# Kernel tuning notes

Measured on AMD Instinct MI355X. Metric: run time of the kernel, lower is better.

The kernel has to match this reference:

```python
import jax, jax.numpy as jnp
import numpy as np

B, T, F, H, OUT = 256, 256, 128, 1024, 128


def setup_inputs() -> dict:
    key = jax.random.key(0)
    ks = jax.random.split(key, 6)
    s_ih = 1.0 / np.sqrt(H)
    return {
        "x": jax.random.normal(ks[0], (B, T, F), dtype=jnp.float32),
        "h0": jnp.zeros((B, H), dtype=jnp.float32),
        "c0": jnp.zeros((B, H), dtype=jnp.float32),
        "W_ih": jax.random.normal(ks[1], (4 * H, F), dtype=jnp.float32) * s_ih,
        "W_hh": jax.random.normal(ks[2], (4 * H, H), dtype=jnp.float32) * s_ih,
        "b_ih": jax.random.normal(ks[3], (4 * H,), dtype=jnp.float32) * s_ih,
        "b_hh": jax.random.normal(ks[4], (4 * H,), dtype=jnp.float32) * s_ih,
        "W_fc": jax.random.normal(ks[5], (OUT, H), dtype=jnp.float32) * s_ih,
        "b_fc": jnp.zeros((OUT,), dtype=jnp.float32),
    }


def _lstm_scan(x, h0, c0, W_ih, W_hh, b_ih, b_hh):
    # Precompute input projections for all timesteps: [T, B, 4H]
    x_t = jnp.swapaxes(x, 0, 1)  # [T, B, F]
    x_proj = jnp.einsum('tbf,gf->tbg', x_t, W_ih) + b_ih + b_hh

    def step(carry, xp):
        h, c = carry
        gates = xp + h @ W_hh.T  # [B, 4H]
        i, f, g, o = jnp.split(gates, 4, axis=-1)  # PyTorch LSTMCell gate order
        i = jax.nn.sigmoid(i)
        f = jax.nn.sigmoid(f)
        g = jnp.tanh(g)
        o = jax.nn.sigmoid(o)
        c = f * c + i * g
        h = o * jnp.tanh(c)
        return (h, c), None

    (h, c), _ = jax.lax.scan(step, (h0, c0), x_proj)
    return h, c


def reference(x, h0, c0, W_ih, W_hh, b_ih, b_hh, W_fc, b_fc):
    h, c = _lstm_scan(x, h0, c0, W_ih, W_hh, b_ih, b_hh)
    sig_out = jax.nn.sigmoid(h)
    # Dropout is identity in eval/reference mode
    return sig_out @ W_fc.T + b_fc  # [B, OUT]
```

## Files before the change

kernel.cpp:

```cpp
#include <hip/hip_runtime.h>


typedef _Float16 f16x8 __attribute__((ext_vector_type(8)));
typedef float f32x4 __attribute__((ext_vector_type(4)));
typedef unsigned long long u64;
typedef unsigned u32;

#define SCOPE_AGENT __HIP_MEMORY_SCOPE_AGENT

#define WS_WP    0ull
#define WS_BIAS  9437184ull
#define WS_XT    (WS_BIAS + 16384ull)
#define WS_HB    (WS_XT + 16777216ull)
#define WS_SIGH  (WS_HB + 1048576ull)
#define WS_BAR   (WS_SIGH + 1048576ull)

__device__ __forceinline__ unsigned short f2h(float f) {
  _Float16 h = (_Float16)f;
  return __builtin_bit_cast(unsigned short, h);
}
__device__ __forceinline__ float fast_sig(float x) {
  return __builtin_amdgcn_rcpf(1.f + __expf(-x));
}
__device__ __forceinline__ float fast_tanh(float x) {
  return __builtin_fmaf(2.f, fast_sig(2.f * x), -1.f);
}
__device__ __forceinline__ unsigned char h_enc(float v) {
  _Float16 gh = (_Float16)(v * 0.00390625f);
  unsigned m = __builtin_bit_cast(unsigned short, gh);
  unsigned r = m + 0x3fu + ((m >> 7) & 1u);
  return (unsigned char)(((m >> 8) & 0x80u) | ((r >> 7) & 0x7fu));
}
__device__ __forceinline__ f16x8 dq(u64 v) {
  unsigned w0 = (unsigned)v, w1 = (unsigned)(v >> 32);
  unsigned e0 = w0 & 0x00ff00ffu, o0 = (w0 >> 8) & 0x00ff00ffu;
  unsigned e1 = w1 & 0x00ff00ffu, o1 = (w1 >> 8) & 0x00ff00ffu;
  int4 t;
  t.x = (int)((e0 + (e0 & 0x00800080u)) << 7);
  t.y = (int)((o0 + (o0 & 0x00800080u)) << 7);
  t.z = (int)((e1 + (e1 & 0x00800080u)) << 7);
  t.w = (int)((o1 + (o1 & 0x00800080u)) << 7);
  return __builtin_bit_cast(f16x8, t);
}
__device__ __forceinline__ void lds_barrier() {
  asm volatile("s_waitcnt lgkmcnt(0)" ::: "memory");
  __builtin_amdgcn_s_barrier();
  asm volatile("" ::: "memory");
}

__global__ void prep_pack(const float* __restrict__ W_ih, const float* __restrict__ W_hh,
                          const float* __restrict__ b_ih, const float* __restrict__ b_hh,
                          unsigned short* __restrict__ wp, float* __restrict__ bias) {
  unsigned i = blockIdx.x * 256u + threadIdx.x;
  if (i < 4718592u) {
    unsigned j = i & 7u;
    unsigned l = (i >> 3) & 63u;
    unsigned rest = i >> 9;
    unsigned q = rest % 9u;
    unsigned rest2 = rest / 9u;
    unsigned ct = rest2 & 7u;
    unsigned rest3 = rest2 >> 3;
    unsigned w = rest3 & 3u;
    unsigned cg = rest3 >> 2;
    unsigned gcol = (ct >> 1) * 1024u + cg * 32u + (ct & 1u) * 16u + (l & 15u);
    unsigned khi = (l >> 4) * 8u;
    float v;
    if (q < 8u) {
      unsigned pj = (0x75643120u >> (4u * j)) & 0xfu;
      unsigned k = w * 256u + q * 32u + khi + pj;
      v = W_hh[(size_t)gcol * 1024u + k];
    } else {
      unsigned f = w * 32u + khi + j;
      v = W_ih[(size_t)gcol * 128u + f];
    }
    wp[i] = f2h(v * 256.0f);
  }
  if (i < 4096u) bias[i] = b_ih[i] + b_hh[i];
}

__global__ void prep_misc(const float* __restrict__ x, const float* __restrict__ h0,
                          unsigned short* __restrict__ xT, unsigned char* __restrict__ hb,
                          unsigned* __restrict__ bar) {
  unsigned i = blockIdx.x * 256u + threadIdx.x;
  if (i < 8388608u) {
    unsigned f = i & 127u;
    unsigned b = (i >> 7) & 255u;
    unsigned t = i >> 15;
    xT[i] = f2h(x[((size_t)b * 256u + t) * 128u + f] * 0.00390625f);
  }
  if (i < 262144u) {
    unsigned col = i & 1023u;
    unsigned grow = i >> 10;
    unsigned g = grow >> 7;
    unsigned rg = (grow >> 4) & 7u;
    unsigned row = grow & 15u;
    hb[((g * 4u + 0u) * 8u + rg) * 16384u + row * 1024u + col] = h_enc(h0[i]);
  }
  if (i < 512u) bar[i] = 0u;
}

#define LOAD_TILE(SA, G, SLOT) do {                                              \
    const char* _b = (const char*)hb + (((G)*4u + (SLOT))*8u + rg)*16384u        \
                     + hi*1024u + w*256u + lo5*8u;                               \
    _Pragma("unroll")                                                            \
    for (int _r = 0; _r < 8; ++_r)                                               \
      SA[_r] = __hip_atomic_load((const u64*)(_b + (unsigned)_r*2048u),          \
                                 __ATOMIC_RELAXED, SCOPE_AGENT);                 \
  } while (0)

__launch_bounds__(256, 1)
__global__ void lstm_main(const unsigned short* __restrict__ wp,
                          const float* __restrict__ bias,
                          const unsigned short* __restrict__ xT,
                          unsigned char* __restrict__ hb,
                          const float* __restrict__ c0,
                          float* __restrict__ sigh,
                          unsigned* __restrict__ bar) {
  extern __shared__ char lds[];
  float4* redv = (float4*)(lds + 16384);
  float*  Sf   = (float*)(lds + 49152);
  unsigned char* hstA = (unsigned char*)(lds + 57344);
  unsigned char* hstB = (unsigned char*)(lds + 57856);

  const unsigned tid = threadIdx.x;
  const unsigned wg  = blockIdx.x;
  const unsigned w   = tid >> 6;
  const unsigned l   = tid & 63u;
  const unsigned rg  = wg >> 5;
  const unsigned cg  = wg & 31u;
  const unsigned lo5 = l & 31u;
  const unsigned hi  = l >> 5;
  const unsigned l15 = l & 15u;
  const unsigned l4  = l >> 4;
  const unsigned row = l4 * 4u + w;

  int4 Braw[8][9];
  {
    const int4* wpv = (const int4*)wp;
    const unsigned wbase = (cg * 4u + w) * 4608u;
#pragma unroll
    for (int ct = 0; ct < 8; ++ct)
#pragma unroll
      for (int q = 0; q < 9; ++q)
        Braw[ct][q] = wpv[wbase + (unsigned)(ct * 9 + q) * 64u + l];
  }

  float bias_v[8];
#pragma unroll
  for (int ct = 0; ct < 8; ++ct)
    bias_v[ct] = bias[(unsigned)(ct >> 1) * 1024u + cg * 32u + (unsigned)(ct & 1) * 16u + l15];

  const unsigned gbA = rg * 16u, gbB = 128u + rg * 16u;
  float cA[2], cB[2];
  unsigned soffA[2], soffB[2];
#pragma unroll
  for (int hh = 0; hh < 2; ++hh) {
    soffA[hh] = (gbA + row) * 1024u + cg * 32u + (unsigned)hh * 16u + l15;
    soffB[hh] = (gbB + row) * 1024u + cg * 32u + (unsigned)hh * 16u + l15;
    cA[hh] = c0[soffA[hh]];
    cB[hh] = c0[soffB[hh]];
  }

  const char* xbase = (const char*)xT;
  const unsigned xoffA = ((gbA + l15) * 128u + w * 32u + l4 * 8u) * 2u;
  const unsigned xoffB = ((gbB + l15) * 128u + w * 32u + l4 * 8u) * 2u;
  unsigned* flags = &bar[rg * 32u];

  const unsigned fragrow = w * 4096u + l15 * 256u;

  u64 saA[8], saB[8];
  int4 xrA, xrB;

  LOAD_TILE(saA, 0u, 0u);
  xrA = *(const int4*)(xbase + xoffA);
  xrB = *(const int4*)(xbase + xoffB);

  for (unsigned t = 0; t < 256u; ++t) {
    const bool last = (t == 255u);
    const unsigned slot = t & 3u, wslot = (t + 1u) & 3u;

#pragma unroll
    for (int r = 0; r < 8; ++r) {
      unsigned rr = hi + 2u * (unsigned)r;
      unsigned d = w * 4096u + rr * 256u + ((lo5 * 8u) ^ ((rr & 15u) << 3));
      *(u64*)(lds + d) = saA[r];
    }
    f32x4 acc[8] = {};
    {
      f16x8 a = __builtin_bit_cast(f16x8, xrA);
#pragma unroll
      for (int ct = 0; ct < 8; ++ct)
        acc[ct] = __builtin_amdgcn_mfma_f32_16x16x32_f16(a, __builtin_bit_cast(f16x8, Braw[ct][8]), acc[ct], 0, 0, 0);
    }
#pragma unroll
    for (int q = 0; q < 8; ++q) {
      unsigned addr = fragrow + (((unsigned)q * 32u + l4 * 8u) ^ (l15 << 3));
      f16x8 a = dq(*(const u64*)(lds + addr));
#pragma unroll
      for (int ct = 0; ct < 8; ++ct)
        acc[ct] = __builtin_amdgcn_mfma_f32_16x16x32_f16(a, __builtin_bit_cast(f16x8, Braw[ct][q]), acc[ct], 0, 0, 0);
    }
    LOAD_TILE(saB, 1u, slot);

#pragma unroll
    for (int ct = 0; ct < 8; ++ct) {
      float4 v; v.x = acc[ct][0]; v.y = acc[ct][1]; v.z = acc[ct][2]; v.w = acc[ct][3];
      redv[(w * 8u + (unsigned)ct) * 64u + l] = v;
    }
    lds_barrier();
#pragma unroll
    for (int c2 = 0; c2 < 2; ++c2) {
      unsigned ct = 2u * w + (unsigned)c2;
      float4 s = redv[ct * 64u + l];
#pragma unroll
      for (int wo = 1; wo < 4; ++wo) {
        float4 v = redv[((unsigned)wo * 8u + ct) * 64u + l];
        s.x += v.x; s.y += v.y; s.z += v.z; s.w += v.w;
      }
      Sf[ct * 256u + 0u * 64u + l] = s.x;
      Sf[ct * 256u + 1u * 64u + l] = s.y;
      Sf[ct * 256u + 2u * 64u + l] = s.z;
      Sf[ct * 256u + 3u * 64u + l] = s.w;
    }
    lds_barrier();
    float gv[8];
#pragma unroll
    for (int ct = 0; ct < 8; ++ct)
      gv[ct] = Sf[(unsigned)ct * 256u + w * 64u + l] + bias_v[ct];
#pragma unroll
    for (int hh = 0; hh < 2; ++hh) {
      float ig = fast_sig(gv[0 * 2 + hh]);
      float fg = fast_sig(gv[1 * 2 + hh]);
      float gg = fast_tanh(gv[2 * 2 + hh]);
      float og = fast_sig(gv[3 * 2 + hh]);
      float cc = fg * cA[hh] + ig * gg;
      cA[hh] = cc;
      float hhv = og * fast_tanh(cc);
      hstA[row * 32u + (unsigned)hh * 16u + l15] = h_enc(hhv);
      if (last) sigh[soffA[hh]] = fast_sig(hhv);
    }
    lds_barrier();
    if (!last && tid < 128u) {
      u32 v = *(const u32*)(hstA + (tid >> 3) * 32u + (tid & 7u) * 4u);
      char* dst = (char*)hb + ((0u * 4u + wslot) * 8u + rg) * 16384u
                  + (tid >> 3) * 1024u + cg * 32u + (tid & 7u) * 4u;
      __hip_atomic_store((u32*)dst, v, __ATOMIC_RELAXED, SCOPE_AGENT);
    }

#pragma unroll
    for (int r = 0; r < 8; ++r) {
      unsigned rr = hi + 2u * (unsigned)r;
      unsigned d = w * 4096u + rr * 256u + ((lo5 * 8u) ^ ((rr & 15u) << 3));
      *(u64*)(lds + d) = saB[r];
    }
    f32x4 accB[8] = {};
    {
      f16x8 a = __builtin_bit_cast(f16x8, xrB);
#pragma unroll
      for (int ct = 0; ct < 8; ++ct)
        accB[ct] = __builtin_amdgcn_mfma_f32_16x16x32_f16(a, __builtin_bit_cast(f16x8, Braw[ct][8]), accB[ct], 0, 0, 0);
    }
#pragma unroll
    for (int q = 0; q < 8; ++q) {
      unsigned addr = fragrow + (((unsigned)q * 32u + l4 * 8u) ^ (l15 << 3));
      f16x8 a = dq(*(const u64*)(lds + addr));
#pragma unroll
      for (int ct = 0; ct < 8; ++ct)
        accB[ct] = __builtin_amdgcn_mfma_f32_16x16x32_f16(a, __builtin_bit_cast(f16x8, Braw[ct][q]), accB[ct], 0, 0, 0);
    }
    if (!last) {
      xrA = *(const int4*)(xbase + xoffA + (t + 1u) * 65536u);
      xrB = *(const int4*)(xbase + xoffB + (t + 1u) * 65536u);
    }

#pragma unroll
    for (int ct = 0; ct < 8; ++ct) {
      float4 v; v.x = accB[ct][0]; v.y = accB[ct][1]; v.z = accB[ct][2]; v.w = accB[ct][3];
      redv[(w * 8u + (unsigned)ct) * 64u + l] = v;
    }
    lds_barrier();
#pragma unroll
    for (int c2 = 0; c2 < 2; ++c2) {
      unsigned ct = 2u * w + (unsigned)c2;
      float4 s = redv[ct * 64u + l];
#pragma unroll
      for (int wo = 1; wo < 4; ++wo) {
        float4 v = redv[((unsigned)wo * 8u + ct) * 64u + l];
        s.x += v.x; s.y += v.y; s.z += v.z; s.w += v.w;
      }
      Sf[ct * 256u + 0u * 64u + l] = s.x;
      Sf[ct * 256u + 1u * 64u + l] = s.y;
      Sf[ct * 256u + 2u * 64u + l] = s.z;
      Sf[ct * 256u + 3u * 64u + l] = s.w;
    }
    lds_barrier();
#pragma unroll
    for (int ct = 0; ct < 8; ++ct)
      gv[ct] = Sf[(unsigned)ct * 256u + w * 64u + l] + bias_v[ct];
#pragma unroll
    for (int hh = 0; hh < 2; ++hh) {
      float ig = fast_sig(gv[0 * 2 + hh]);
      float fg = fast_sig(gv[1 * 2 + hh]);
      float gg = fast_tanh(gv[2 * 2 + hh]);
      float og = fast_sig(gv[3 * 2 + hh]);
      float cc = fg * cB[hh] + ig * gg;
      cB[hh] = cc;
      float hhv = og * fast_tanh(cc);
      hstB[row * 32u + (unsigned)hh * 16u + l15] = h_enc(hhv);
      if (last) sigh[soffB[hh]] = fast_sig(hhv);
    }
    lds_barrier();
    if (!last) {
      if (tid < 128u) {
        u32 v = *(const u32*)(hstB + (tid >> 3) * 32u + (tid & 7u) * 4u);
        char* dst = (char*)hb + ((1u * 4u + wslot) * 8u + rg) * 16384u
                    + (tid >> 3) * 1024u + cg * 32u + (tid & 7u) * 4u;
        __hip_atomic_store((u32*)dst, v, __ATOMIC_RELAXED, SCOPE_AGENT);
      }
      __syncthreads();
      if (tid == 0)
        __hip_atomic_store(&flags[cg], t + 1u, __ATOMIC_RELAXED, SCOPE_AGENT);
      {
        const unsigned tgt = t + 1u;
        for (;;) {
          unsigned f = __hip_atomic_load(&flags[w * 8u + (l & 7u)],
                                         __ATOMIC_RELAXED, SCOPE_AGENT);
          if (__all(f >= tgt)) break;
          __builtin_amdgcn_s_sleep(1);
        }
      }
      LOAD_TILE(saA, 0u, wslot);
    }
  }
}

__global__ void final_fc(const float* __restrict__ sigh, const float* __restrict__ W_fc,
                         const float* __restrict__ b_fc, float* __restrict__ out) {
  unsigned b = blockIdx.x;
  unsigned o = threadIdx.x;
  const float* hrow = sigh + (size_t)b * 1024u;
  const float* wrow = W_fc + (size_t)o * 1024u;
  float acc = b_fc[o];
#pragma unroll 8
  for (unsigned k = 0; k < 1024u; k += 4u) {
    float4 hv = *(const float4*)(hrow + k);
    float4 wv = *(const float4*)(wrow + k);
    acc += hv.x * wv.x + hv.y * wv.y + hv.z * wv.z + hv.w * wv.w;
  }
  out[b * 128u + o] = acc;
}

extern "C" void kernel_launch(void* const* d_in, const int* in_sizes, int n_in,
                              void* d_out, int out_size, void* d_ws, size_t ws_size,
                              hipStream_t stream) {
  (void)in_sizes; (void)n_in; (void)out_size; (void)ws_size;
  const float* x    = (const float*)d_in[0];
  const float* h0   = (const float*)d_in[1];
  const float* c0   = (const float*)d_in[2];
  const float* W_ih = (const float*)d_in[3];
  const float* W_hh = (const float*)d_in[4];
  const float* b_ih = (const float*)d_in[5];
  const float* b_hh = (const float*)d_in[6];
  const float* W_fc = (const float*)d_in[7];
  const float* b_fc = (const float*)d_in[8];

  char* ws = (char*)d_ws;
  unsigned short* wp   = (unsigned short*)(ws + WS_WP);
  float*          bias = (float*)(ws + WS_BIAS);
  unsigned short* xT   = (unsigned short*)(ws + WS_XT);
  unsigned char*  hb   = (unsigned char*)(ws + WS_HB);
  float*          sigh = (float*)(ws + WS_SIGH);
  unsigned*       bar  = (unsigned*)(ws + WS_BAR);
  float*          out  = (float*)d_out;

  prep_pack<<<18432, 256, 0, stream>>>(W_ih, W_hh, b_ih, b_hh, wp, bias);
  prep_misc<<<32768, 256, 0, stream>>>(x, h0, xT, hb, bar);
  lstm_main<<<256, 256, 58368, stream>>>(wp, bias, xT, hb, c0, sigh, bar);
  final_fc<<<256, 128, 0, stream>>>(sigh, W_fc, b_fc, out);
}
```

Baseline: 1.506 ms.

## Split grid barrier into per-half flags so each batch half syncs independently

Replaces the single per-step all-group barrier with two flag sets, one per batch half (A and B). Each half now waits only on its own producers: A's h tile is polled after B's h is published, and B's tile is polled at the top of the next step. This lets one half's barrier wait overlap with the other half's compute. The cost is an extra polling loop and extra LDS barriers per step, plus more complex ordering of the relaxed-atomic handoff between the two halves.

```diff
diff --git a/kernel.cpp b/kernel.cpp
--- a/kernel.cpp
+++ b/kernel.cpp
@@ -108,6 +108,15 @@
                                  __ATOMIC_RELAXED, SCOPE_AGENT);                 \
   } while (0)
 
+#define POLL(FL, TGT) do {                                                       \
+    for (;;) {                                                                   \
+      unsigned _f = __hip_atomic_load((FL) + w*8u + (l & 7u),                    \
+                                      __ATOMIC_RELAXED, SCOPE_AGENT);            \
+      if (__all(_f >= (TGT))) break;                                             \
+      __builtin_amdgcn_s_sleep(1);                                               \
+    }                                                                            \
+  } while (0)
+
 __launch_bounds__(256, 1)
 __global__ void lstm_main(const unsigned short* __restrict__ wp,
                           const float* __restrict__ bias,
@@ -164,7 +173,8 @@
   const char* xbase = (const char*)xT;
   const unsigned xoffA = ((gbA + l15) * 128u + w * 32u + l4 * 8u) * 2u;
   const unsigned xoffB = ((gbB + l15) * 128u + w * 32u + l4 * 8u) * 2u;
-  unsigned* flags = &bar[rg * 32u];
+  unsigned* flagsA = &bar[rg * 32u];
+  unsigned* flagsB = &bar[256u + rg * 32u];
 
   const unsigned fragrow = w * 4096u + l15 * 256u;
 
@@ -178,6 +188,9 @@
   for (unsigned t = 0; t < 256u; ++t) {
     const bool last = (t == 255u);
     const unsigned slot = t & 3u, wslot = (t + 1u) & 3u;
+
+    POLL(flagsB, t);
+    LOAD_TILE(saB, 1u, slot);
 
 #pragma unroll
     for (int r = 0; r < 8; ++r) {
@@ -185,6 +198,8 @@
       unsigned d = w * 4096u + rr * 256u + ((lo5 * 8u) ^ ((rr & 15u) << 3));
       *(u64*)(lds + d) = saA[r];
     }
+    lds_barrier();
+
     f32x4 acc[8] = {};
     {
       f16x8 a = __builtin_bit_cast(f16x8, xrA);
@@ -200,7 +215,6 @@
       for (int ct = 0; ct < 8; ++ct)
         acc[ct] = __builtin_amdgcn_mfma_f32_16x16x32_f16(a, __builtin_bit_cast(f16x8, Braw[ct][q]), acc[ct], 0, 0, 0);
     }
-    LOAD_TILE(saB, 1u, slot);
 
 #pragma unroll
     for (int ct = 0; ct < 8; ++ct) {
@@ -253,6 +267,8 @@
       unsigned d = w * 4096u + rr * 256u + ((lo5 * 8u) ^ ((rr & 15u) << 3));
       *(u64*)(lds + d) = saB[r];
     }
+    lds_barrier();
+
     f32x4 accB[8] = {};
     {
       f16x8 a = __builtin_bit_cast(f16x8, xrB);
@@ -268,17 +284,15 @@
       for (int ct = 0; ct < 8; ++ct)
         accB[ct] = __builtin_amdgcn_mfma_f32_16x16x32_f16(a, __builtin_bit_cast(f16x8, Braw[ct][q]), accB[ct], 0, 0, 0);
     }
-    if (!last) {
-      xrA = *(const int4*)(xbase + xoffA + (t + 1u) * 65536u);
-      xrB = *(const int4*)(xbase + xoffB + (t + 1u) * 65536u);
-    }
-
 #pragma unroll
     for (int ct = 0; ct < 8; ++ct) {
       float4 v; v.x = accB[ct][0]; v.y = accB[ct][1]; v.z = accB[ct][2]; v.w = accB[ct][3];
       redv[(w * 8u + (unsigned)ct) * 64u + l] = v;
     }
-    lds_barrier();
+    __syncthreads();
+    if (!last && tid == 0)
+      __hip_atomic_store(&flagsA[cg], t + 1u, __ATOMIC_RELAXED, SCOPE_AGENT);
+
 #pragma unroll
     for (int c2 = 0; c2 < 2; ++c2) {
       unsigned ct = 2u * w + (unsigned)c2;
@@ -310,6 +324,7 @@
       if (last) sigh[soffB[hh]] = fast_sig(hhv);
     }
     lds_barrier();
+
     if (!last) {
       if (tid < 128u) {
         u32 v = *(const u32*)(hstB + (tid >> 3) * 32u + (tid & 7u) * 4u);
@@ -317,19 +332,13 @@
                     + (tid >> 3) * 1024u + cg * 32u + (tid & 7u) * 4u;
         __hip_atomic_store((u32*)dst, v, __ATOMIC_RELAXED, SCOPE_AGENT);
       }
-      __syncthreads();
+      POLL(flagsA, t + 1u);
+      LOAD_TILE(saA, 0u, wslot);
+      xrA = *(const int4*)(xbase + xoffA + (t + 1u) * 65536u);
+      xrB = *(const int4*)(xbase + xoffB + (t + 1u) * 65536u);
+      lds_barrier();
       if (tid == 0)
-        __hip_atomic_store(&flags[cg], t + 1u, __ATOMIC_RELAXED, SCOPE_AGENT);
-      {
-        const unsigned tgt = t + 1u;
-        for (;;) {
-          unsigned f = __hip_atomic_load(&flags[w * 8u + (l & 7u)],
-                                         __ATOMIC_RELAXED, SCOPE_AGENT);
-          if (__all(f >= tgt)) break;
-          __builtin_amdgcn_s_sleep(1);
-        }
-      }
-      LOAD_TILE(saA, 0u, wslot);
+        __hip_atomic_store(&flagsB[cg], t + 1u, __ATOMIC_RELAXED, SCOPE_AGENT);
     }
   }
 }
```

After: 1.588 ms. +5.4%, slower.
